# Kernel optimization log

Measured on AMD Instinct MI355X. Metric: run time of the kernel, lower is better.

Reference implementation:

```python
import jax, jax.numpy as jnp
import numpy as np

K = 32
TEMP = 0.01
OTHERWEIGHT = 0.5
BS = 64
F = 128


def setup_inputs() -> dict:
    key = jax.random.key(0)
    k1, k2, k3 = jax.random.split(key, 3)
    feats1 = jax.random.normal(k1, (K * BS, F), dtype=jnp.float32)
    feats2 = jax.random.normal(k2, (K * BS, F), dtype=jnp.float32)
    overlap_inds = jax.random.randint(k3, (K,), 0, 2).astype(bool)
    return {"feats1": feats1, "feats2": feats2, "overlap_inds": overlap_inds, "bs": BS}


def _labels(overlap_inds, bs):
    k = overlap_inds.shape[0]
    labels1 = jnp.repeat(jnp.arange(k), bs)
    nov = (~overlap_inds).astype(jnp.int32)
    excl_nov = jnp.cumsum(nov) - nov  # exclusive count of non-overlaps before i
    class2 = jnp.where(overlap_inds, jnp.arange(k), k + excl_nov)
    labels2 = jnp.repeat(class2, bs)
    return jnp.concatenate([labels1, labels2])


def reference(feats1, feats2, overlap_inds, bs):
    n1 = feats1.shape[0]
    labels = _labels(overlap_inds, bs)            # [n]
    feats = jnp.concatenate([feats1, feats2])     # [n, F]
    n = feats.shape[0]

    logits = (feats @ feats.T) * TEMP             # [n, n]; log of exp(sim*temp)
    sim = jnp.exp(logits)

    same = labels[:, None] == labels[None, :]
    eye = jnp.eye(n, dtype=bool)
    pos_mask = same & ~eye
    neg_mask = ~same

    is2 = jnp.arange(n) >= n1                     # second-view block indicator
    cross_w = jnp.where(is2[:, None] != is2[None, :], OTHERWEIGHT, 1.0)

    neg_sum = jnp.sum(jnp.where(neg_mask, sim, 0.0), axis=1)      # [n]
    # -log(pos / neg_sum) = log(neg_sum) - logits
    per_pair_loss = cross_w * (jnp.log(neg_sum)[:, None] - logits)
    total_loss = jnp.sum(jnp.where(pos_mask, per_pair_loss, 0.0))
    total_pos = jnp.sum(pos_mask)

    # accuracy: a positive pair counts iff its sim beats ALL negatives in its row
    max_neg = jnp.max(jnp.where(neg_mask, sim, -jnp.inf), axis=1)  # [n]
    correct = pos_mask & (sim > max_neg[:, None])
    acc = jnp.sum(correct).astype(jnp.float32) / total_pos.astype(jnp.float32)

    loss = total_loss / total_pos.astype(jnp.float32)
    return acc, loss
```

## Files before the change

### kernel.cpp

```cpp
#include <hip/hip_runtime.h>
#include <math.h>

#define TEMP 0.01f

typedef __attribute__((ext_vector_type(8))) short short8;
typedef __attribute__((ext_vector_type(4))) float f32x4;
typedef __attribute__((ext_vector_type(4))) unsigned short ushort4_t;


__device__ __forceinline__ unsigned bf16_hi_bits(float x) {
  unsigned u = __float_as_uint(x);
  return (u + 0x7FFFu + ((u >> 16) & 1u)) >> 16;
}

struct HL { unsigned short h, l; };

__device__ __forceinline__ HL split1(float x) {
  unsigned hb = bf16_hi_bits(x);
  float hf = __uint_as_float(hb << 16);
  unsigned lb = bf16_hi_bits(x - hf);
  HL r;
  r.h = (unsigned short)hb;
  r.l = (unsigned short)lb;
  return r;
}

__device__ __forceinline__ void decode_ov(const int* __restrict__ ov_raw,
                                          int* s_class2, int* s_v2b,
                                          int* s_ov) {
  const int t = threadIdx.x;
  if (t < 64) {
    int v = (t < 32) ? ov_raw[t] : 0;
    bool valid = (t >= 32) || (v == 0) || (v == 1);
    unsigned long long okmask = __ballot(valid);
    bool as_int = (okmask == ~0ull);
    s_v2b[t] = 0;
    if (t < 32) {
      int o = as_int ? v : (((const unsigned char*)ov_raw)[t] ? 1 : 0);
      s_ov[t] = o;
      unsigned long long nz = __ballot((t < 32) && !o);
      int cum = __popcll(nz & ((1ull << t) - 1ull));
      int c2 = o ? t : 32 + cum;
      s_class2[t] = c2;
      s_v2b[c2] = t;
    }
  }
}

__device__ __forceinline__ int labf(int g, const int* s_class2) {
  return (g < 2048) ? (g >> 6) : s_class2[(g - 2048) >> 6];
}

__device__ __forceinline__ int slotf(int g, int cls, const int* s_v2b) {
  if (g < 2048) return g - (cls << 6);
  return ((cls < 32) ? 64 : 0) + (g - 2048 - (s_v2b[cls] << 6));
}

__global__ __launch_bounds__(256, 2) void main_kernel(
    const float* __restrict__ f1, const float* __restrict__ f2,
    const int* __restrict__ ov_raw, float* __restrict__ nsum,
    int* __restrict__ nmaxb, float* __restrict__ pcw,
    float* __restrict__ pcwl, float* __restrict__ posbuf) {
  __shared__ unsigned short Ah[128][64], Al[128][64];
  __shared__ unsigned short Bh[128][64], Bl[128][64];
  __shared__ int s_class2[32], s_v2b[64], s_ov[32];

  decode_ov(ov_raw, s_class2, s_v2b, s_ov);

  const int tt = blockIdx.x;
  int bi = (int)(32.5f - sqrtf(1056.25f - 2.0f * (float)tt));
  while (bi * 32 - bi * (bi - 1) / 2 > tt) --bi;
  while ((bi + 1) * 32 - (bi + 1) * bi / 2 <= tt) ++bi;
  const int bj = bi + (tt - (bi * 32 - bi * (bi - 1) / 2));
  const bool off = (bi != bj);

  const int ibase = bi * 128, jbase = bj * 128;
  const float* asrc = (ibase < 2048) ? (f1 + (size_t)ibase * 128)
                                     : (f2 + (size_t)(ibase - 2048) * 128);
  const float* bsrc = (jbase < 2048) ? (f1 + (size_t)jbase * 128)
                                     : (f2 + (size_t)(jbase - 2048) * 128);
  const int t = threadIdx.x;
  const int l = t & 63;
  const int wid = t >> 6;
  const int wy = wid >> 1, wx = wid & 1;
  const int rr = l & 15;
  const int q = l >> 4;
  const int sw = l & 7;

  f32x4 acc[4][4];
#pragma unroll
  for (int mi = 0; mi < 4; ++mi)
#pragma unroll
    for (int ni = 0; ni < 4; ++ni) acc[mi][ni] = (f32x4)0.0f;

  const int kq = t & 15;
  const int r0 = t >> 4;
  const int stc = ((kq >> 1) ^ (r0 & 7)) * 8 + (kq & 1) * 4;

  for (int kc = 0; kc < 2; ++kc) {
    if (kc) __syncthreads();
#pragma unroll
    for (int p = 0; p < 8; ++p) {
      const int r = r0 + 16 * p;
      const float4 va = *(const float4*)(asrc + (size_t)r * 128 + kc * 64 + kq * 4);
      const float4 vb = *(const float4*)(bsrc + (size_t)r * 128 + kc * 64 + kq * 4);
      ushort4_t ha, la, hb, lb;
      HL s;
      s = split1(va.x); ha.x = s.h; la.x = s.l;
      s = split1(va.y); ha.y = s.h; la.y = s.l;
      s = split1(va.z); ha.z = s.h; la.z = s.l;
      s = split1(va.w); ha.w = s.h; la.w = s.l;
      s = split1(vb.x); hb.x = s.h; lb.x = s.l;
      s = split1(vb.y); hb.y = s.h; lb.y = s.l;
      s = split1(vb.z); hb.z = s.h; lb.z = s.l;
      s = split1(vb.w); hb.w = s.h; lb.w = s.l;
      *(ushort4_t*)&Ah[r][stc] = ha;
      *(ushort4_t*)&Al[r][stc] = la;
      *(ushort4_t*)&Bh[r][stc] = hb;
      *(ushort4_t*)&Bl[r][stc] = lb;
    }
    __syncthreads();

#pragma unroll
    for (int s = 0; s < 2; ++s) {
      const int pb = ((((s << 2) | q)) ^ sw) << 3;
      short8 afh[4], afl[4], bfh[4], bfl[4];
#pragma unroll
      for (int mi = 0; mi < 4; ++mi) {
        const int ar = wy * 64 + mi * 16 + rr;
        afh[mi] = *(const short8*)&Ah[ar][pb];
        afl[mi] = *(const short8*)&Al[ar][pb];
        const int br = wx * 64 + mi * 16 + rr;
        bfh[mi] = *(const short8*)&Bh[br][pb];
        bfl[mi] = *(const short8*)&Bl[br][pb];
      }
#pragma unroll
      for (int mi = 0; mi < 4; ++mi)
#pragma unroll
        for (int ni = 0; ni < 4; ++ni) {
          acc[mi][ni] = __builtin_amdgcn_mfma_f32_16x16x32_bf16(
              afh[mi], bfh[ni], acc[mi][ni], 0, 0, 0);
          acc[mi][ni] = __builtin_amdgcn_mfma_f32_16x16x32_bf16(
              afh[mi], bfl[ni], acc[mi][ni], 0, 0, 0);
          acc[mi][ni] = __builtin_amdgcn_mfma_f32_16x16x32_bf16(
              afl[mi], bfh[ni], acc[mi][ni], 0, 0, 0);
        }
    }
  }

  const float cw = ((ibase < 2048) != (jbase < 2048)) ? 0.5f : 1.0f;
  int gj[4], lj[4];
#pragma unroll
  for (int ni = 0; ni < 4; ++ni) {
    gj[ni] = jbase + wx * 64 + ni * 16 + rr;
    lj[ni] = labf(gj[ni], s_class2);
  }

  float cnsum[4], cnmax[4], cpcw[4], cpcwl[4];
#pragma unroll
  for (int ni = 0; ni < 4; ++ni) {
    cnsum[ni] = 0.f; cnmax[ni] = 0.f; cpcw[ni] = 0.f; cpcwl[ni] = 0.f;
  }

#pragma unroll
  for (int mi = 0; mi < 4; ++mi) {
#pragma unroll
    for (int reg = 0; reg < 4; ++reg) {
      const int gi = ibase + wy * 64 + mi * 16 + q * 4 + reg;
      const int li = labf(gi, s_class2);
      float rnsum = 0.f, rnmax = 0.f, rpcw = 0.f, rpcwl = 0.f;
#pragma unroll
      for (int ni = 0; ni < 4; ++ni) {
        const int gjj = gj[ni];
        if (gi == gjj) continue;
        const float logit = acc[mi][ni][reg] * TEMP;
        const float e = __expf(logit);
        if (li == lj[ni]) {
          rpcw += cw;
          rpcwl += cw * logit;
          posbuf[(size_t)gi * 128 + slotf(gjj, li, s_v2b)] = e;
          if (off) {
            cpcw[ni] += cw;
            cpcwl[ni] += cw * logit;
            posbuf[(size_t)gjj * 128 + slotf(gi, li, s_v2b)] = e;
          }
        } else {
          rnsum += e;
          rnmax = fmaxf(rnmax, e);
          if (off) {
            cnsum[ni] += e;
            cnmax[ni] = fmaxf(cnmax[ni], e);
          }
        }
      }
#pragma unroll
      for (int m = 1; m < 16; m <<= 1) {
        rnsum += __shfl_xor(rnsum, m, 64);
        rpcw  += __shfl_xor(rpcw, m, 64);
        rpcwl += __shfl_xor(rpcwl, m, 64);
        rnmax = fmaxf(rnmax, __shfl_xor(rnmax, m, 64));
      }
      if (rr == 0) {
        atomicAdd(&nsum[gi], rnsum);
        atomicAdd(&pcw[gi], rpcw);
        atomicAdd(&pcwl[gi], rpcwl);
        atomicMax(&nmaxb[gi], __float_as_int(rnmax));
      }
    }
  }

  if (off) {
#pragma unroll
    for (int ni = 0; ni < 4; ++ni) {
      float cs = cnsum[ni], cm = cnmax[ni], cp = cpcw[ni], cl = cpcwl[ni];
#pragma unroll
      for (int m = 16; m < 64; m <<= 1) {
        cs += __shfl_xor(cs, m, 64);
        cp += __shfl_xor(cp, m, 64);
        cl += __shfl_xor(cl, m, 64);
        cm = fmaxf(cm, __shfl_xor(cm, m, 64));
      }
      if (q == 0) {
        const int g = gj[ni];
        atomicAdd(&nsum[g], cs);
        atomicAdd(&pcw[g], cp);
        atomicAdd(&pcwl[g], cl);
        atomicMax(&nmaxb[g], __float_as_int(cm));
      }
    }
  }
}

__global__ __launch_bounds__(256) void finalize_kernel(
    const int* __restrict__ ov_raw, const float* __restrict__ nsum,
    const int* __restrict__ nmaxb, const float* __restrict__ pcw,
    const float* __restrict__ pcwl, const float* __restrict__ posbuf,
    float* __restrict__ accum, int* __restrict__ counter,
    float* __restrict__ out) {
  __shared__ int s_class2[32], s_v2b[64], s_ov[32];
  __shared__ float sc[4], sp[4], sl[4];
  decode_ov(ov_raw, s_class2, s_v2b, s_ov);
  __syncthreads();

  const int t = threadIdx.x;
  const int w = t >> 6, lane = t & 63;
  float cnt_acc = 0.f, pos_acc = 0.f, loss_acc = 0.f;
  const int rbase = blockIdx.x * 64 + w * 16;
  for (int i = 0; i < 16; ++i) {
    const int row = rbase + i;
    const float2 pv = *(const float2*)&posbuf[(size_t)row * 128 + lane * 2];
    const int c = labf(row, s_class2);
    const int size = (c < 32) ? (s_ov[c] ? 128 : 64) : 64;
    int selfslot;
    if (row < 2048) selfslot = row - (c << 6);
    else selfslot = ((c < 32) ? 64 : 0) + (row - 2048 - (s_v2b[c] << 6));
    const float nmax = __int_as_float(nmaxb[row]);
    const int s0 = lane * 2;
    int h = 0;
    if (s0 < size && s0 != selfslot && pv.x > nmax) h++;
    if (s0 + 1 < size && s0 + 1 != selfslot && pv.y > nmax) h++;
    cnt_acc += (float)h;
    if (lane == 0) {
      loss_acc += logf(nsum[row]) * pcw[row] - pcwl[row];
      pos_acc += (float)(size - 1);
    }
  }
#pragma unroll
  for (int m = 1; m < 64; m <<= 1) {
    cnt_acc += __shfl_xor(cnt_acc, m, 64);
    pos_acc += __shfl_xor(pos_acc, m, 64);
    loss_acc += __shfl_xor(loss_acc, m, 64);
  }
  if (lane == 0) { sc[w] = cnt_acc; sp[w] = pos_acc; sl[w] = loss_acc; }
  __syncthreads();
  if (t == 0) {
    atomicAdd(&accum[0], sc[0] + sc[1] + sc[2] + sc[3]);
    atomicAdd(&accum[1], sp[0] + sp[1] + sp[2] + sp[3]);
    atomicAdd(&accum[2], sl[0] + sl[1] + sl[2] + sl[3]);
    __threadfence();
    const int prev = atomicAdd(counter, 1);
    if (prev == 63) {
      const float c = atomicAdd(&accum[0], 0.0f);
      const float tp = atomicAdd(&accum[1], 0.0f);
      const float lo = atomicAdd(&accum[2], 0.0f);
      out[0] = c / tp;
      out[1] = lo / tp;
    }
  }
}

extern "C" void kernel_launch(void* const* d_in, const int* in_sizes, int n_in,
                              void* d_out, int out_size, void* d_ws,
                              size_t ws_size, hipStream_t stream) {
  const float* f1 = (const float*)d_in[0];
  const float* f2 = (const float*)d_in[1];
  const int* ov = (const int*)d_in[2];
  float* out = (float*)d_out;

  float* wsf = (float*)d_ws;
  int* wsi = (int*)d_ws;
  float* nsum   = wsf;
  int* nmaxb    = wsi + 4096;
  float* pcw    = wsf + 8192;
  float* pcwl   = wsf + 12288;
  float* accum  = wsf + 16384;
  int* counter  = wsi + 16387;
  float* posbuf = wsf + 16400;

  (void)hipMemsetAsync(nsum, 0, (size_t)16392 * sizeof(float), stream);

  main_kernel<<<528, 256, 0, stream>>>(f1, f2, ov, nsum, nmaxb, pcw, pcwl,
                                       posbuf);
  finalize_kernel<<<64, 256, 0, stream>>>(ov, nsum, nmaxb, pcw, pcwl, posbuf,
                                          accum, counter, out);
}
```

Baseline: 108.1 us.

## Precompute bf16 hi/lo split once and reuse across tiles; pair diagonal tiles

Adds a precompute kernel that splits all features into swizzled bf16 high and low halves once in workspace, so each main-kernel tile copies ready-made halves instead of reconverting fp32 inputs. Diagonal tiles load only the A operand and read B fragments from it. Two diagonal tiles are packed per block, giving 512 blocks instead of 528 to even out work. It costs an extra kernel launch, an extra round trip to global memory, and a second pass of the tile code inside diagonal blocks.

Result: slower. 111.4 us (+3.0%).

```diff
diff --git a/kernel.cpp b/kernel.cpp
--- a/kernel.cpp
+++ b/kernel.cpp
@@ -5,7 +5,7 @@
 
 typedef __attribute__((ext_vector_type(8))) short short8;
 typedef __attribute__((ext_vector_type(4))) float f32x4;
-typedef __attribute__((ext_vector_type(4))) unsigned short ushort4_t;
+typedef __attribute__((ext_vector_type(8))) unsigned short ushort8_t;
 
 
 __device__ __forceinline__ unsigned bf16_hi_bits(float x) {
@@ -56,29 +56,41 @@
   return ((cls < 32) ? 64 : 0) + (g - 2048 - (s_v2b[cls] << 6));
 }
 
-__global__ __launch_bounds__(256, 2) void main_kernel(
+__global__ __launch_bounds__(256) void precompute_kernel(
     const float* __restrict__ f1, const float* __restrict__ f2,
-    const int* __restrict__ ov_raw, float* __restrict__ nsum,
-    int* __restrict__ nmaxb, float* __restrict__ pcw,
-    float* __restrict__ pcwl, float* __restrict__ posbuf) {
-  __shared__ unsigned short Ah[128][64], Al[128][64];
-  __shared__ unsigned short Bh[128][64], Bl[128][64];
-  __shared__ int s_class2[32], s_v2b[64], s_ov[32];
-
-  decode_ov(ov_raw, s_class2, s_v2b, s_ov);
-
-  const int tt = blockIdx.x;
-  int bi = (int)(32.5f - sqrtf(1056.25f - 2.0f * (float)tt));
-  while (bi * 32 - bi * (bi - 1) / 2 > tt) --bi;
-  while ((bi + 1) * 32 - (bi + 1) * bi / 2 <= tt) ++bi;
-  const int bj = bi + (tt - (bi * 32 - bi * (bi - 1) / 2));
-  const bool off = (bi != bj);
-
-  const int ibase = bi * 128, jbase = bj * 128;
-  const float* asrc = (ibase < 2048) ? (f1 + (size_t)ibase * 128)
-                                     : (f2 + (size_t)(ibase - 2048) * 128);
-  const float* bsrc = (jbase < 2048) ? (f1 + (size_t)jbase * 128)
-                                     : (f2 + (size_t)(jbase - 2048) * 128);
+    unsigned short* __restrict__ Ph, unsigned short* __restrict__ Pl) {
+  const int u = blockIdx.x * 256 + threadIdx.x;
+  const int row = u >> 4;
+  const int gid = u & 15;
+  const int kc = gid >> 3, P = gid & 7;
+  const int k = kc * 64 + (P ^ (row & 7)) * 8;
+  const float* src = (row < 2048) ? (f1 + (size_t)row * 128)
+                                  : (f2 + (size_t)(row - 2048) * 128);
+  const float4 a = *(const float4*)(src + k);
+  const float4 b = *(const float4*)(src + k + 4);
+  ushort8_t hi, lo;
+  HL s;
+  s = split1(a.x); hi.s0 = s.h; lo.s0 = s.l;
+  s = split1(a.y); hi.s1 = s.h; lo.s1 = s.l;
+  s = split1(a.z); hi.s2 = s.h; lo.s2 = s.l;
+  s = split1(a.w); hi.s3 = s.h; lo.s3 = s.l;
+  s = split1(b.x); hi.s4 = s.h; lo.s4 = s.l;
+  s = split1(b.y); hi.s5 = s.h; lo.s5 = s.l;
+  s = split1(b.z); hi.s6 = s.h; lo.s6 = s.l;
+  s = split1(b.w); hi.s7 = s.h; lo.s7 = s.l;
+  *(ushort8_t*)&Ph[(size_t)row * 128 + gid * 8] = hi;
+  *(ushort8_t*)&Pl[(size_t)row * 128 + gid * 8] = lo;
+}
+
+__device__ __forceinline__ void compute_tile(
+    int ibase, int jbase, bool diag,
+    const unsigned short* __restrict__ Ph, const unsigned short* __restrict__ Pl,
+    unsigned short (*Ah)[64], unsigned short (*Al)[64],
+    unsigned short (*Bh)[64], unsigned short (*Bl)[64],
+    const int* s_class2, const int* s_v2b,
+    float* __restrict__ nsum, int* __restrict__ nmaxb,
+    float* __restrict__ pcw, float* __restrict__ pcwl,
+    float* __restrict__ posbuf) {
   const int t = threadIdx.x;
   const int l = t & 63;
   const int wid = t >> 6;
@@ -93,31 +105,26 @@
 #pragma unroll
     for (int ni = 0; ni < 4; ++ni) acc[mi][ni] = (f32x4)0.0f;
 
-  const int kq = t & 15;
-  const int r0 = t >> 4;
-  const int stc = ((kq >> 1) ^ (r0 & 7)) * 8 + (kq & 1) * 4;
+  const int gg = t & 7;
+  const int r0 = t >> 3;
 
   for (int kc = 0; kc < 2; ++kc) {
-    if (kc) __syncthreads();
-#pragma unroll
-    for (int p = 0; p < 8; ++p) {
-      const int r = r0 + 16 * p;
-      const float4 va = *(const float4*)(asrc + (size_t)r * 128 + kc * 64 + kq * 4);
-      const float4 vb = *(const float4*)(bsrc + (size_t)r * 128 + kc * 64 + kq * 4);
-      ushort4_t ha, la, hb, lb;
-      HL s;
-      s = split1(va.x); ha.x = s.h; la.x = s.l;
-      s = split1(va.y); ha.y = s.h; la.y = s.l;
-      s = split1(va.z); ha.z = s.h; la.z = s.l;
-      s = split1(va.w); ha.w = s.h; la.w = s.l;
-      s = split1(vb.x); hb.x = s.h; lb.x = s.l;
-      s = split1(vb.y); hb.y = s.h; lb.y = s.l;
-      s = split1(vb.z); hb.z = s.h; lb.z = s.l;
-      s = split1(vb.w); hb.w = s.h; lb.w = s.l;
-      *(ushort4_t*)&Ah[r][stc] = ha;
-      *(ushort4_t*)&Al[r][stc] = la;
-      *(ushort4_t*)&Bh[r][stc] = hb;
-      *(ushort4_t*)&Bl[r][stc] = lb;
+    __syncthreads();
+#pragma unroll
+    for (int p = 0; p < 4; ++p) {
+      const int r = r0 + 32 * p;
+      const size_t arec = (size_t)(ibase + r) * 128 + kc * 64 + gg * 8;
+      const ushort8_t vah = *(const ushort8_t*)&Ph[arec];
+      const ushort8_t val = *(const ushort8_t*)&Pl[arec];
+      *(ushort8_t*)&Ah[r][gg * 8] = vah;
+      *(ushort8_t*)&Al[r][gg * 8] = val;
+      if (!diag) {
+        const size_t brec = (size_t)(jbase + r) * 128 + kc * 64 + gg * 8;
+        const ushort8_t vbh = *(const ushort8_t*)&Ph[brec];
+        const ushort8_t vbl = *(const ushort8_t*)&Pl[brec];
+        *(ushort8_t*)&Bh[r][gg * 8] = vbh;
+        *(ushort8_t*)&Bl[r][gg * 8] = vbl;
+      }
     }
     __syncthreads();
 
@@ -131,8 +138,10 @@
         afh[mi] = *(const short8*)&Ah[ar][pb];
         afl[mi] = *(const short8*)&Al[ar][pb];
         const int br = wx * 64 + mi * 16 + rr;
-        bfh[mi] = *(const short8*)&Bh[br][pb];
-        bfl[mi] = *(const short8*)&Bl[br][pb];
+        bfh[mi] = diag ? *(const short8*)&Ah[br][pb]
+                       : *(const short8*)&Bh[br][pb];
+        bfl[mi] = diag ? *(const short8*)&Al[br][pb]
+                       : *(const short8*)&Bl[br][pb];
       }
 #pragma unroll
       for (int mi = 0; mi < 4; ++mi)
@@ -148,6 +157,7 @@
     }
   }
 
+  const bool off = !diag;
   const float cw = ((ibase < 2048) != (jbase < 2048)) ? 0.5f : 1.0f;
   int gj[4], lj[4];
 #pragma unroll
@@ -231,6 +241,33 @@
   }
 }
 
+__global__ __launch_bounds__(256, 2) void main_kernel(
+    const unsigned short* __restrict__ Ph, const unsigned short* __restrict__ Pl,
+    const int* __restrict__ ov_raw, float* __restrict__ nsum,
+    int* __restrict__ nmaxb, float* __restrict__ pcw,
+    float* __restrict__ pcwl, float* __restrict__ posbuf) {
+  __shared__ unsigned short Ah[128][64], Al[128][64];
+  __shared__ unsigned short Bh[128][64], Bl[128][64];
+  __shared__ int s_class2[32], s_v2b[64], s_ov[32];
+
+  decode_ov(ov_raw, s_class2, s_v2b, s_ov);
+
+  const int bid = blockIdx.x;
+  if (bid < 496) {
+    int idx = bid, bi = 0;
+    while (idx >= 31 - bi) { idx -= 31 - bi; ++bi; }
+    const int bj = bi + 1 + idx;
+    compute_tile(bi * 128, bj * 128, false, Ph, Pl, Ah, Al, Bh, Bl, s_class2,
+                 s_v2b, nsum, nmaxb, pcw, pcwl, posbuf);
+  } else {
+    const int d = (bid - 496) * 2;
+    compute_tile(d * 128, d * 128, true, Ph, Pl, Ah, Al, Bh, Bl, s_class2,
+                 s_v2b, nsum, nmaxb, pcw, pcwl, posbuf);
+    compute_tile((d + 1) * 128, (d + 1) * 128, true, Ph, Pl, Ah, Al, Bh, Bl,
+                 s_class2, s_v2b, nsum, nmaxb, pcw, pcwl, posbuf);
+  }
+}
+
 __global__ __launch_bounds__(256) void finalize_kernel(
     const int* __restrict__ ov_raw, const float* __restrict__ nsum,
     const int* __restrict__ nmaxb, const float* __restrict__ pcw,
@@ -306,10 +343,13 @@
   float* accum  = wsf + 16384;
   int* counter  = wsi + 16387;
   float* posbuf = wsf + 16400;
+  unsigned short* Ph = (unsigned short*)(wsf + 540688);
+  unsigned short* Pl = Ph + 524288;
 
   (void)hipMemsetAsync(nsum, 0, (size_t)16392 * sizeof(float), stream);
 
-  main_kernel<<<528, 256, 0, stream>>>(f1, f2, ov, nsum, nmaxb, pcw, pcwl,
+  precompute_kernel<<<256, 256, 0, stream>>>(f1, f2, Ph, Pl);
+  main_kernel<<<512, 256, 0, stream>>>(Ph, Pl, ov, nsum, nmaxb, pcw, pcwl,
                                        posbuf);
   finalize_kernel<<<64, 256, 0, stream>>>(ov, nsum, nmaxb, pcw, pcwl, posbuf,
                                           accum, counter, out);
```
